# Kernel optimization log

Hardware: AMD Instinct MI355X
Metric: run time of the kernel (lower is better)

The kernel has to match this reference:

```python
import jax, jax.numpy as jnp
import numpy as np
from functools import partial

P = 7          # cfg.POOLING_SIZE
SAMP = 2       # fixed sampling ratio (torchvision sampling_ratio=0 is adaptive; fixed 2 used for jit)
IM_H, IM_W = 800.0, 1216.0


def conv2d(x, w, b, pad):
    y = jax.lax.conv_general_dilated(
        x, w, window_strides=(1, 1), padding=[(pad, pad), (pad, pad)],
        dimension_numbers=("NCHW", "OIHW", "NCHW"))
    return y + b[None, :, None, None]


def upsample_add(x, y):
    # F.upsample(x, size=(H,W), mode='bilinear') + y  (align_corners=False / half-pixel)
    return jax.image.resize(x, y.shape, method="bilinear") + y


def roi_align_level(feat, rois, scale):
    """torchvision roi_align (aligned=False) of all rois on one feature map.
    feat: [B,C,H,W]; rois: [N,5] = (batch_idx, x1,y1,x2,y2) in image coords.
    Returns [N,C,P,P]."""
    B, C, H, W = feat.shape
    Hf, Wf = float(H), float(W)

    def one(roi):
        b = roi[0].astype(jnp.int32)
        img = jnp.take(feat, b, axis=0)                       # [C,H,W]
        x1, y1, x2, y2 = roi[1] * scale, roi[2] * scale, roi[3] * scale, roi[4] * scale
        rw = jnp.maximum(x2 - x1, 1.0)
        rh = jnp.maximum(y2 - y1, 1.0)
        bh, bw = rh / P, rw / P
        # sample coords per bin: [P, SAMP] -> flat [P*SAMP]
        ys = (y1 + jnp.arange(P, dtype=feat.dtype)[:, None] * bh
              + (jnp.arange(SAMP, dtype=feat.dtype)[None, :] + 0.5) * bh / SAMP).reshape(-1)
        xs = (x1 + jnp.arange(P, dtype=feat.dtype)[:, None] * bw
              + (jnp.arange(SAMP, dtype=feat.dtype)[None, :] + 0.5) * bw / SAMP).reshape(-1)
        vy = (ys >= -1.0) & (ys <= Hf)
        vx = (xs >= -1.0) & (xs <= Wf)
        yc = jnp.clip(ys, 0.0, Hf - 1.0)
        xc = jnp.clip(xs, 0.0, Wf - 1.0)
        y0 = jnp.floor(yc).astype(jnp.int32)
        x0 = jnp.floor(xc).astype(jnp.int32)
        y1i = jnp.minimum(y0 + 1, H - 1)
        x1i = jnp.minimum(x0 + 1, W - 1)
        ly = yc - y0.astype(feat.dtype)
        lx = xc - x0.astype(feat.dtype)
        hy, hx = 1.0 - ly, 1.0 - lx
        v00 = img[:, y0[:, None], x0[None, :]]                # [C, PS, PS]
        v01 = img[:, y0[:, None], x1i[None, :]]
        v10 = img[:, y1i[:, None], x0[None, :]]
        v11 = img[:, y1i[:, None], x1i[None, :]]
        val = (hy[:, None] * hx[None, :]) * v00 + (hy[:, None] * lx[None, :]) * v01 \
            + (ly[:, None] * hx[None, :]) * v10 + (ly[:, None] * lx[None, :]) * v11
        val = val * (vy[:, None] & vx[None, :]).astype(feat.dtype)
        return val.reshape(C, P, SAMP, P, SAMP).mean(axis=(2, 4))   # [C,P,P]

    return jax.vmap(one)(rois)


def setup_inputs() -> dict:
    key = jax.random.key(0)
    ks = jax.random.split(key, 24)
    B = 2
    c2 = jax.random.normal(ks[0], (B, 256, 200, 304), jnp.float32)
    c3 = jax.random.normal(ks[1], (B, 512, 100, 152), jnp.float32)
    c4 = jax.random.normal(ks[2], (B, 1024, 50, 76), jnp.float32)
    c5 = jax.random.normal(ks[3], (B, 2048, 25, 38), jnp.float32)
    # FPN params (all project to 256 channels)
    def w(k, o, i, s):
        return jax.random.normal(k, (o, i, s, s), jnp.float32) * 0.01
    w_top, b_top = w(ks[4], 256, 2048, 1), jnp.zeros((256,), jnp.float32)
    w_lat1, b_lat1 = w(ks[5], 256, 1024, 1), jnp.zeros((256,), jnp.float32)
    w_lat2, b_lat2 = w(ks[6], 256, 512, 1), jnp.zeros((256,), jnp.float32)
    w_lat3, b_lat3 = w(ks[7], 256, 256, 1), jnp.zeros((256,), jnp.float32)
    w_sm1, b_sm1 = w(ks[8], 256, 256, 3), jnp.zeros((256,), jnp.float32)
    w_sm2, b_sm2 = w(ks[9], 256, 256, 3), jnp.zeros((256,), jnp.float32)
    w_sm3, b_sm3 = w(ks[10], 256, 256, 3), jnp.zeros((256,), jnp.float32)
    # ROIs: batch idx + boxes with log-uniform sizes spanning pyramid levels 2..5
    N = 1024
    bidx = jax.random.randint(ks[11], (N,), 0, B).astype(jnp.float32)
    size = jnp.exp(jax.random.uniform(ks[12], (N,), jnp.float32,
                                      np.log(32.0), np.log(640.0)))
    ar = jnp.exp(jax.random.uniform(ks[13], (N,), jnp.float32,
                                    np.log(0.5), np.log(2.0)))
    bw_ = jnp.minimum(size * jnp.sqrt(ar), IM_W - 1)
    bh_ = jnp.minimum(size / jnp.sqrt(ar), IM_H - 1)
    x1 = jax.random.uniform(ks[14], (N,), jnp.float32) * (IM_W - bw_)
    y1 = jax.random.uniform(ks[15], (N,), jnp.float32) * (IM_H - bh_)
    rois = jnp.stack([bidx, x1, y1, x1 + bw_, y1 + bh_], axis=1)
    im_info = jnp.array([[IM_H, IM_W, 1.0]], jnp.float32)
    return dict(c2=c2, c3=c3, c4=c4, c5=c5, rois=rois, im_info=im_info,
                w_top=w_top, b_top=b_top, w_lat1=w_lat1, b_lat1=b_lat1,
                w_lat2=w_lat2, b_lat2=b_lat2, w_lat3=w_lat3, b_lat3=b_lat3,
                w_sm1=w_sm1, b_sm1=b_sm1, w_sm2=w_sm2, b_sm2=b_sm2,
                w_sm3=w_sm3, b_sm3=b_sm3)


def reference(c2, c3, c4, c5, rois, im_info,
              w_top, b_top, w_lat1, b_lat1, w_lat2, b_lat2, w_lat3, b_lat3,
              w_sm1, b_sm1, w_sm2, b_sm2, w_sm3, b_sm3):
    # --- FPN top-down pathway ---
    p5 = conv2d(c5, w_top, b_top, 0)
    p4 = conv2d(upsample_add(p5, conv2d(c4, w_lat1, b_lat1, 0)), w_sm1, b_sm1, 1)
    p3 = conv2d(upsample_add(p4, conv2d(c3, w_lat2, b_lat2, 0)), w_sm2, b_sm2, 1)
    p2 = conv2d(upsample_add(p3, conv2d(c2, w_lat3, b_lat3, 0)), w_sm3, b_sm3, 1)
    mrcnn_feats = [p2, p3, p4, p5]
    # --- _PyramidRoI_Feat (POOLING_MODE == 'align') ---
    h = rois[:, 4] - rois[:, 2] + 1.0
    w_ = rois[:, 3] - rois[:, 1] + 1.0
    lvl = jnp.round(jnp.log(jnp.sqrt(h * w_) / 224.0) + 4.0)
    lvl = jnp.clip(lvl, 2.0, 5.0)
    im_h = im_info[0, 0]
    N, C = rois.shape[0], p2.shape[1]
    out = jnp.zeros((N, C, P, P), p2.dtype)
    for i, l in enumerate(range(2, 6)):
        scale = mrcnn_feats[i].shape[2] / im_h
        feat_l = roi_align_level(mrcnn_feats[i], rois, scale)
        out = jnp.where((lvl == l)[:, None, None, None], feat_l, out)
    return out
```

## Files before the change

### kernel.cpp

```cpp
#include <hip/hip_runtime.h>
#include <math.h>

typedef __attribute__((ext_vector_type(8))) short short8;
typedef __attribute__((ext_vector_type(4))) float f32x4;
typedef __attribute__((ext_vector_type(8))) unsigned short ushort8v;

__device__ __forceinline__ ushort f2bf(float f) {
    unsigned u = __builtin_bit_cast(unsigned, f);
    u = (u + 0x7fffu + ((u >> 16) & 1u)) >> 16;
    return (ushort)u;
}
__device__ __forceinline__ float bf2f(ushort h) {
    unsigned u = ((unsigned)h) << 16;
    return __builtin_bit_cast(float, u);
}

__device__ __forceinline__ void cp16(const ushort* g, ushort* l) {
    __builtin_amdgcn_global_load_lds(
        (const __attribute__((address_space(1))) unsigned int*)g,
        (__attribute__((address_space(3))) unsigned int*)l, 16, 0, 0);
}

__device__ __forceinline__ void pair_decode(int bid, int nt, int& tile, int& mm) {
    int f16 = (nt * 2) & ~15;
    if (bid < f16) { tile = ((bid >> 4) << 3) | (bid & 7); mm = (bid >> 3) & 1; }
    else { int r = bid - f16; tile = (f16 >> 1) + (r >> 1); mm = r & 1; }
}


__global__ void nchw2nhwc(const float* __restrict__ in, ushort* __restrict__ out,
                          int C, int HW)
{
    __shared__ float tile[32][33];
    const int n  = blockIdx.z;
    const int c0 = blockIdx.y * 32;
    const int p0 = blockIdx.x * 32;
    const float* inp = in + (size_t)n * C * HW;
    ushort* op = out + (size_t)n * HW * C;
    const int tx = threadIdx.x & 31, ty = threadIdx.x >> 5;
    #pragma unroll
    for (int i = 0; i < 4; ++i) {
        int c = ty + i * 8;
        int p = p0 + tx;
        tile[c][tx] = (p < HW) ? inp[(size_t)(c0 + c) * HW + p] : 0.f;
    }
    __syncthreads();
    #pragma unroll
    for (int i = 0; i < 4; ++i) {
        int p = ty + i * 8;
        if (p0 + p < HW) op[(size_t)(p0 + p) * C + c0 + tx] = f2bf(tile[tx][p]);
    }
}

__global__ void cast_k(const float* __restrict__ in, ushort* __restrict__ out, int n)
{
    int i = blockIdx.x * 256 + threadIdx.x;
    if (i < n) out[i] = f2bf(in[i]);
}

__global__ void pack_w3(const float* __restrict__ w, ushort* __restrict__ wp, int Cin)
{
    int i = blockIdx.x * 256 + threadIdx.x;
    int total = 256 * Cin * 9;
    if (i >= total) return;
    int co  = i / (9 * Cin);
    int rem = i - co * 9 * Cin;
    int tap = rem / Cin;
    int ci  = rem - tap * Cin;
    wp[i] = f2bf(w[(size_t)co * Cin * 9 + (size_t)ci * 9 + tap]);
}

__global__ void zero_border(ushort* __restrict__ T, int Hp, int Wp, int NB, int total)
{
    int i = blockIdx.x * 256 + threadIdx.x;
    if (i >= total) return;
    const int cg = (i & 31) * 8;
    const int pb = i >> 5;
    const int n  = pb / NB;
    const int b  = pb - n * NB;
    int y, x;
    if (b < 2 * Wp) { y = (b < Wp) ? 0 : (Hp - 1); x = (b < Wp) ? b : (b - Wp); }
    else { int rem = b - 2 * Wp; y = 1 + (rem >> 1); x = (rem & 1) ? (Wp - 1) : 0; }
    ushort8v z = {0, 0, 0, 0, 0, 0, 0, 0};
    *(ushort8v*)&T[((size_t)n * Hp * Wp + (size_t)y * Wp + x) * 256 + cg] = z;
}

template<int PADOUT>
__global__ __launch_bounds__(256, 4) void conv1_mfma(
    const ushort* __restrict__ X, const ushort* __restrict__ Wt,
    const float* __restrict__ bias, ushort* __restrict__ Y,
    int Cin, int H, int Wd, int nP)
{
    const int HW = H * Wd;
    int tile, mm;
    pair_decode(blockIdx.x, nP, tile, mm);
    const int p0 = tile * 128;
    const int m0 = mm << 7;
    const int n  = blockIdx.z;
    const ushort* Xn = X + (size_t)n * HW * Cin;

    const int t    = threadIdx.x;
    const int lane = t & 63;
    const int wave = t >> 6;
    const int l15  = lane & 15, lq = lane >> 4;

    __shared__ __align__(16) ushort smem[17408];

    const int rA  = ((t >> 6) << 4) | (t & 15);
    const int lq8 = ((t >> 4) & 3) * 8;
    const ushort* agA = Wt + (size_t)(m0 + rA) * Cin + lq8;
    const ushort* agB = agA + (size_t)64 * Cin;
    const ushort* XqA = Xn + (size_t)(p0 + rA) * Cin + lq8;
    const ushort* XqB = Xn + (size_t)(p0 + rA + 64) * Cin + lq8;

    const int fr    = (lq * 16 + l15) * 8;
    const int aoff  = ((wave >> 1) * 4) * 512;
    const int boff  = 4096 + ((wave & 1) * 4) * 512;
    const int wbase = wave << 9;

    const int nch = Cin >> 5;

    auto stage = [&](int bb, int c) {
        const int kA = c << 5;
        cp16(agA + kA, &smem[bb + wbase]);
        cp16(agB + kA, &smem[bb + 2048 + wbase]);
        cp16(XqA + kA, &smem[bb + 4096 + wbase]);
        cp16(XqB + kA, &smem[bb + 6144 + wbase]);
    };

    f32x4 acc[4][4] = {};

    stage(0, 0);
    __syncthreads();

    #pragma unroll 1
    for (int c = 0; c < nch; c += 2) {
        {
            stage(8192, c + 1);
            short8 af[4], bf[4];
            #pragma unroll
            for (int mi = 0; mi < 4; ++mi) af[mi] = *(const short8*)&smem[aoff + mi * 512 + fr];
            #pragma unroll
            for (int ni = 0; ni < 4; ++ni) bf[ni] = *(const short8*)&smem[boff + ni * 512 + fr];
            #pragma unroll
            for (int mi = 0; mi < 4; ++mi)
                #pragma unroll
                for (int ni = 0; ni < 4; ++ni)
                    acc[mi][ni] = __builtin_amdgcn_mfma_f32_16x16x32_bf16(
                        af[mi], bf[ni], acc[mi][ni], 0, 0, 0);
            __syncthreads();
        }
        {
            if (c + 2 < nch) stage(0, c + 2);
            short8 af[4], bf[4];
            #pragma unroll
            for (int mi = 0; mi < 4; ++mi) af[mi] = *(const short8*)&smem[8192 + aoff + mi * 512 + fr];
            #pragma unroll
            for (int ni = 0; ni < 4; ++ni) bf[ni] = *(const short8*)&smem[8192 + boff + ni * 512 + fr];
            #pragma unroll
            for (int mi = 0; mi < 4; ++mi)
                #pragma unroll
                for (int ni = 0; ni < 4; ++ni)
                    acc[mi][ni] = __builtin_amdgcn_mfma_f32_16x16x32_bf16(
                        af[mi], bf[ni], acc[mi][ni], 0, 0, 0);
            __syncthreads();
        }
    }

    const int wm = (wave >> 1) * 64, wn = (wave & 1) * 64;
    #pragma unroll
    for (int mi = 0; mi < 4; ++mi) {
        const int co = wm + mi * 16 + lq * 4;
        float4 bv = *(const float4*)&bias[m0 + co];
        float bb4[4] = {bv.x, bv.y, bv.z, bv.w};
        #pragma unroll
        for (int ni = 0; ni < 4; ++ni) {
            const int p = wn + ni * 16 + l15;
            ushort4 h;
            h.x = f2bf(acc[mi][ni][0] + bb4[0]);
            h.y = f2bf(acc[mi][ni][1] + bb4[1]);
            h.z = f2bf(acc[mi][ni][2] + bb4[2]);
            h.w = f2bf(acc[mi][ni][3] + bb4[3]);
            *(ushort4*)&smem[p * 136 + co] = h;
        }
    }
    __syncthreads();

    ushort* Yn = PADOUT ? (Y + (size_t)n * (H + 2) * (Wd + 2) * 256)
                        : (Y + (size_t)n * HW * 256);
    #pragma unroll
    for (int it = 0; it < 8; ++it) {
        int idx = it * 256 + t;
        int px  = idx >> 4;
        int off = (idx & 15) * 8;
        int qq  = p0 + px;
        if (qq >= HW) continue;
        uint4 v = *(const uint4*)&smem[px * 136 + off];
        if (PADOUT) {
            int y = qq / Wd, x = qq - (qq / Wd) * Wd;
            *(uint4*)&Yn[((size_t)(y + 1) * (Wd + 2) + (x + 1)) * 256 + m0 + off] = v;
        } else {
            *(uint4*)&Yn[(size_t)qq * 256 + m0 + off] = v;
        }
    }
}

__global__ __launch_bounds__(256, 4) void conv3_mfma(
    const ushort* __restrict__ X, const ushort* __restrict__ Wt,
    const float* __restrict__ bias, ushort* __restrict__ Y,
    int Hout, int Wout, int ct, int nt)
{
    const int Wp = Wout + 2;
    int tile, mm;
    pair_decode(blockIdx.x, nt, tile, mm);
    const int ty = tile / ct, tx = tile - ty * ct;
    int y0 = ty * 8;  if (y0 > Hout - 8)  y0 = Hout - 8;
    int x0 = tx * 16; if (x0 > Wout - 16) x0 = Wout - 16;
    const int m0 = mm << 7;
    const int nb = blockIdx.z;
    const ushort* Xn = X + (size_t)nb * (Hout + 2) * Wp * 256;

    const int t    = threadIdx.x;
    const int lane = t & 63;
    const int wave = t >> 6;
    const int l15  = lane & 15, lq = lane >> 4;

    __shared__ __align__(16) ushort smem[19712];
    const int A0o = 0, A1o = 4096, B0o = 8192, B1o = 13952;

    const int rA  = ((t >> 6) << 4) | (t & 15);
    const int lq8 = ((t >> 4) & 3) * 8;
    const ushort* agA = Wt + (size_t)(m0 + rA) * 2304 + lq8;
    const ushort* agB = agA + (size_t)64 * 2304;

    const int fr   = (lq * 16 + l15) * 8;
    const int aoff = (wave >> 1) * 2048;
    const int bb   = (((wave & 1) * 16 + lq) * 144) + l15 * 8;

    auto stageA = [&](int ab, int cc, int tap) {
        const int kA = tap * 256 + (cc << 5);
        cp16(agA + kA, &smem[ab + t * 8]);
        cp16(agB + kA, &smem[ab + 2048 + t * 8]);
    };
    auto stageB = [&](int bbuf, int cc) {
        const int cb = cc << 5;
        #pragma unroll
        for (int rnd = 0; rnd < 3; ++rnd) {
            int s = rnd * 256 + t;
            if (s < 720) {
                int py  = s / 72, rem = s - py * 72;
                int lqq = rem / 18, pxc = rem - lqq * 18;
                cp16(Xn + ((size_t)(y0 + py) * Wp + (x0 + pxc)) * 256 + cb + lqq * 8,
                     &smem[bbuf + s * 8]);
            }
        }
    };

    f32x4 acc[4][4] = {};

    stageB(B0o, 0);
    stageA(A0o, 0, 0);
    __syncthreads();

    #pragma unroll 1
    for (int cc = 0; cc < 8; ++cc) {
        const int pb = cc & 1;
        const int Bb = pb ? B1o : B0o;
        #pragma unroll
        for (int tap = 0; tap < 9; ++tap) {
            const int pa = pb ^ (tap & 1);
            const int Ab = pa ? A1o : A0o;
            const int An = pa ? A0o : A1o;
            if (tap < 8) stageA(An, cc, tap + 1);
            else if (cc < 7) { stageB(pb ? B0o : B1o, cc + 1); stageA(An, cc + 1, 0); }
            const int dy = tap / 3, dx = tap - dy * 3;
            short8 af[4], bf[4];
            #pragma unroll
            for (int mi = 0; mi < 4; ++mi) af[mi] = *(const short8*)&smem[Ab + aoff + mi * 512 + fr];
            #pragma unroll
            for (int ni = 0; ni < 4; ++ni) bf[ni] = *(const short8*)&smem[Bb + bb + (ni + dy) * 576 + dx * 8];
            #pragma unroll
            for (int mi = 0; mi < 4; ++mi)
                #pragma unroll
                for (int ni = 0; ni < 4; ++ni)
                    acc[mi][ni] = __builtin_amdgcn_mfma_f32_16x16x32_bf16(
                        af[mi], bf[ni], acc[mi][ni], 0, 0, 0);
            __syncthreads();
        }
    }

    const int wm = (wave >> 1) * 64, wn = (wave & 1) * 64;
    #pragma unroll
    for (int mi = 0; mi < 4; ++mi) {
        const int co = wm + mi * 16 + lq * 4;
        float4 bv = *(const float4*)&bias[m0 + co];
        float bb4[4] = {bv.x, bv.y, bv.z, bv.w};
        #pragma unroll
        for (int ni = 0; ni < 4; ++ni) {
            const int p = wn + ni * 16 + l15;
            ushort4 h;
            h.x = f2bf(acc[mi][ni][0] + bb4[0]);
            h.y = f2bf(acc[mi][ni][1] + bb4[1]);
            h.z = f2bf(acc[mi][ni][2] + bb4[2]);
            h.w = f2bf(acc[mi][ni][3] + bb4[3]);
            *(ushort4*)&smem[p * 136 + co] = h;
        }
    }
    __syncthreads();

    ushort* Yn = Y + (size_t)nb * Hout * Wout * 256;
    #pragma unroll
    for (int it = 0; it < 8; ++it) {
        int idx = it * 256 + t;
        int p   = idx >> 4;
        int off = (idx & 15) * 8;
        int yy  = y0 + (p >> 4), xx = x0 + (p & 15);
        *(uint4*)&Yn[((size_t)yy * Wout + xx) * 256 + m0 + off] =
            *(const uint4*)&smem[p * 136 + off];
    }
}

__global__ void upsample_add_nhwc(ushort* __restrict__ T, const ushort* __restrict__ Pn,
                                  int H, int Wd, int total32)
{
    int i = blockIdx.x * 256 + threadIdx.x;
    if (i >= total32) return;
    const int cg = (i & 31) * 8;
    const int q  = i >> 5;
    const int HW = H * Wd;
    const int n   = q / HW;
    const int pix = q - n * HW;
    const int y = pix / Wd, x = pix - (pix / Wd) * Wd;
    const int Hh = H >> 1, Wh = Wd >> 1;

    float sy = fminf(fmaxf(y * 0.5f - 0.25f, 0.f), (float)(Hh - 1));
    float sx = fminf(fmaxf(x * 0.5f - 0.25f, 0.f), (float)(Wh - 1));
    int y0 = (int)sy, x0 = (int)sx;
    int y1 = min(y0 + 1, Hh - 1), x1 = min(x0 + 1, Wh - 1);
    float fy = sy - (float)y0, fx = sx - (float)x0;

    const ushort* base = Pn + (size_t)n * Hh * Wh * 256 + cg;
    ushort8v a00 = *(const ushort8v*)&base[(size_t)(y0 * Wh + x0) * 256];
    ushort8v a01 = *(const ushort8v*)&base[(size_t)(y0 * Wh + x1) * 256];
    ushort8v a10 = *(const ushort8v*)&base[(size_t)(y1 * Wh + x0) * 256];
    ushort8v a11 = *(const ushort8v*)&base[(size_t)(y1 * Wh + x1) * 256];

    const int Wp2 = Wd + 2;
    ushort* tp = T + ((size_t)n * (H + 2) * Wp2 + (size_t)(y + 1) * Wp2 + (x + 1)) * 256 + cg;
    ushort8v tv = *(ushort8v*)tp;
    ushort8v r;
    #pragma unroll
    for (int j = 0; j < 8; ++j) {
        float v = (1.f - fy) * ((1.f - fx) * bf2f(a00[j]) + fx * bf2f(a01[j]))
                +        fy  * ((1.f - fx) * bf2f(a10[j]) + fx * bf2f(a11[j]));
        r[j] = f2bf(bf2f(tv[j]) + v);
    }
    *(ushort8v*)tp = r;
}

__global__ __launch_bounds__(256) void roi_align_k(
    const float* __restrict__ rois, const float* __restrict__ im_info,
    const ushort* __restrict__ p2, const ushort* __restrict__ p3,
    const ushort* __restrict__ p4, const ushort* __restrict__ p5,
    float* __restrict__ out)
{
    const int r   = blockIdx.x;
    const int tid = threadIdx.x;

    __shared__ int   s_y0[14], s_y1[14], s_x0[14], s_x1[14];
    __shared__ float s_ly[14], s_lx[14], s_vy[14], s_vx[14];
    __shared__ float s_o[256 * 49];

    const float bx  = rois[r * 5 + 0];
    const float x1r = rois[r * 5 + 1];
    const float y1r = rois[r * 5 + 2];
    const float x2r = rois[r * 5 + 3];
    const float y2r = rois[r * 5 + 4];

    const float hh = y2r - y1r + 1.f;
    const float ww = x2r - x1r + 1.f;
    float lf = rintf(logf(sqrtf(hh * ww) * (1.f / 224.f)) + 4.f);
    lf = fminf(fmaxf(lf, 2.f), 5.f);
    const int lvl = (int)lf;

    const ushort* feat; int H, W;
    if      (lvl == 2) { feat = p2; H = 200; W = 304; }
    else if (lvl == 3) { feat = p3; H = 100; W = 152; }
    else if (lvl == 4) { feat = p4; H = 50;  W = 76;  }
    else               { feat = p5; H = 25;  W = 38;  }

    const float im_h  = im_info[0];
    const float scale = (float)H / im_h;
    const float x1 = x1r * scale, y1 = y1r * scale;
    const float x2 = x2r * scale, y2 = y2r * scale;
    const float rw = fmaxf(x2 - x1, 1.f);
    const float rh = fmaxf(y2 - y1, 1.f);
    const float bh = rh * (1.f / 7.f);
    const float bw = rw * (1.f / 7.f);

    if (tid < 28) {
        if (tid < 14) {
            int i = tid, pi = i >> 1, s = i & 1;
            float ys = y1 + pi * bh + (s + 0.5f) * bh * 0.5f;
            float v  = (ys >= -1.f && ys <= (float)H) ? 1.f : 0.f;
            float yc = fminf(fmaxf(ys, 0.f), (float)H - 1.f);
            int y0 = (int)floorf(yc);
            s_y0[i] = y0; s_y1[i] = min(y0 + 1, H - 1);
            s_ly[i] = yc - (float)y0; s_vy[i] = v;
        } else {
            int i = tid - 14, pi = i >> 1, s = i & 1;
            float xs = x1 + pi * bw + (s + 0.5f) * bw * 0.5f;
            float v  = (xs >= -1.f && xs <= (float)W) ? 1.f : 0.f;
            float xc = fminf(fmaxf(xs, 0.f), (float)W - 1.f);
            int x0 = (int)floorf(xc);
            s_x0[i] = x0; s_x1[i] = min(x0 + 1, W - 1);
            s_lx[i] = xc - (float)x0; s_vx[i] = v;
        }
    }
    __syncthreads();

    const int b = (int)bx;
    const ushort* fc = feat + (size_t)b * H * W * 256 + tid;

    #pragma unroll
    for (int py = 0; py < 7; ++py) {
        #pragma unroll
        for (int px = 0; px < 7; ++px) {
            float acc = 0.f;
            #pragma unroll
            for (int sy = 0; sy < 2; ++sy) {
                #pragma unroll
                for (int sx = 0; sx < 2; ++sx) {
                    int iy = py * 2 + sy, ix = px * 2 + sx;
                    float ly = s_ly[iy], lx = s_lx[ix];
                    float hy = 1.f - ly, hx = 1.f - lx;
                    int y0 = s_y0[iy], y1i = s_y1[iy];
                    int x0 = s_x0[ix], x1i = s_x1[ix];
                    float v00 = bf2f(fc[(size_t)(y0 * W + x0) * 256]);
                    float v01 = bf2f(fc[(size_t)(y0 * W + x1i) * 256]);
                    float v10 = bf2f(fc[(size_t)(y1i * W + x0) * 256]);
                    float v11 = bf2f(fc[(size_t)(y1i * W + x1i) * 256]);
                    float val = hy * hx * v00 + hy * lx * v01
                              + ly * hx * v10 + ly * lx * v11;
                    acc += val * s_vy[iy] * s_vx[ix];
                }
            }
            s_o[tid * 49 + py * 7 + px] = acc * 0.25f;
        }
    }
    __syncthreads();
    float* orow = out + (size_t)r * 256 * 49;
    for (int it = 0; it < 49; ++it)
        orow[it * 256 + tid] = s_o[it * 256 + tid];
}

static inline int cdiv(int a, int b) { return (a + b - 1) / b; }

extern "C" void kernel_launch(void* const* d_in, const int* in_sizes, int n_in,
                              void* d_out, int out_size, void* d_ws, size_t ws_size,
                              hipStream_t stream) {
    const float* c2      = (const float*)d_in[0];
    const float* c3      = (const float*)d_in[1];
    const float* c4      = (const float*)d_in[2];
    const float* c5      = (const float*)d_in[3];
    const float* rois    = (const float*)d_in[4];
    const float* im_info = (const float*)d_in[5];
    const float* w_top   = (const float*)d_in[6];
    const float* b_top   = (const float*)d_in[7];
    const float* w_lat1  = (const float*)d_in[8];
    const float* b_lat1  = (const float*)d_in[9];
    const float* w_lat2  = (const float*)d_in[10];
    const float* b_lat2  = (const float*)d_in[11];
    const float* w_lat3  = (const float*)d_in[12];
    const float* b_lat3  = (const float*)d_in[13];
    const float* w_sm1   = (const float*)d_in[14];
    const float* b_sm1   = (const float*)d_in[15];
    const float* w_sm2   = (const float*)d_in[16];
    const float* b_sm2   = (const float*)d_in[17];
    const float* w_sm3   = (const float*)d_in[18];
    const float* b_sm3   = (const float*)d_in[19];
    float* out = (float*)d_out;
    ushort* ws = (ushort*)d_ws;

    ushort* c2t = ws;
    ushort* c3t = c2t + 31129600;
    ushort* c4t = c3t + 15564800;
    ushort* c5t = c4t + 7782400;
    ushort* p5  = c5t + 3891200;
    ushort* p4  = p5  + 486400;
    ushort* p3  = p4  + 1945600;
    ushort* T   = p3  + 7782400;
    ushort* wtp = T   + 31647744;
    ushort* wl1 = wtp + 524288;
    ushort* wl2 = wl1 + 262144;
    ushort* wl3 = wl2 + 131072;
    ushort* ws1 = wl3 + 65536;
    ushort* ws2 = ws1 + 589824;
    ushort* ws3 = ws2 + 589824;
    ushort* p2  = c2t;

    dim3 blk(256);

    cast_k<<<cdiv(524288, 256), blk, 0, stream>>>(w_top,  wtp, 524288);
    cast_k<<<cdiv(262144, 256), blk, 0, stream>>>(w_lat1, wl1, 262144);
    cast_k<<<cdiv(131072, 256), blk, 0, stream>>>(w_lat2, wl2, 131072);
    cast_k<<<cdiv(65536,  256), blk, 0, stream>>>(w_lat3, wl3, 65536);
    pack_w3<<<cdiv(589824, 256), blk, 0, stream>>>(w_sm1, ws1, 256);
    pack_w3<<<cdiv(589824, 256), blk, 0, stream>>>(w_sm2, ws2, 256);
    pack_w3<<<cdiv(589824, 256), blk, 0, stream>>>(w_sm3, ws3, 256);

    nchw2nhwc<<<dim3(1900, 8,  2), blk, 0, stream>>>(c2, c2t, 256,  60800);
    nchw2nhwc<<<dim3(475, 16,  2), blk, 0, stream>>>(c3, c3t, 512,  15200);
    nchw2nhwc<<<dim3(119, 32,  2), blk, 0, stream>>>(c4, c4t, 1024, 3800);
    nchw2nhwc<<<dim3(30,  64,  2), blk, 0, stream>>>(c5, c5t, 2048, 950);

    conv1_mfma<0><<<dim3(16, 1, 2), blk, 0, stream>>>(c5t, wtp, b_top, p5, 2048, 25, 38, 8);

    conv1_mfma<1><<<dim3(60, 1, 2), blk, 0, stream>>>(c4t, wl1, b_lat1, T, 1024, 50, 76, 30);
    zero_border<<<cdiv(16384, 256), blk, 0, stream>>>(T, 52, 78, 256, 16384);
    upsample_add_nhwc<<<cdiv(2 * 3800 * 32, 256), blk, 0, stream>>>(T, p5, 50, 76, 2 * 3800 * 32);
    conv3_mfma<<<dim3(70, 1, 2), blk, 0, stream>>>(T, ws1, b_sm1, p4, 50, 76, 5, 35);

    conv1_mfma<1><<<dim3(238, 1, 2), blk, 0, stream>>>(c3t, wl2, b_lat2, T, 512, 100, 152, 119);
    zero_border<<<cdiv(32512, 256), blk, 0, stream>>>(T, 102, 154, 508, 32512);
    upsample_add_nhwc<<<cdiv(2 * 15200 * 32, 256), blk, 0, stream>>>(T, p4, 100, 152, 2 * 15200 * 32);
    conv3_mfma<<<dim3(260, 1, 2), blk, 0, stream>>>(T, ws2, b_sm2, p3, 100, 152, 10, 130);

    conv1_mfma<1><<<dim3(950, 1, 2), blk, 0, stream>>>(c2t, wl3, b_lat3, T, 256, 200, 304, 475);
    zero_border<<<cdiv(64768, 256), blk, 0, stream>>>(T, 202, 306, 1012, 64768);
    upsample_add_nhwc<<<cdiv(2 * 60800 * 32, 256), blk, 0, stream>>>(T, p3, 200, 304, 2 * 60800 * 32);
    conv3_mfma<<<dim3(950, 1, 2), blk, 0, stream>>>(T, ws3, b_sm3, p2, 200, 304, 19, 475);

    roi_align_k<<<dim3(1024), blk, 0, stream>>>(rois, im_info, p2, p3, p4, p5, out);
}
```

Measured before the change: 1.024 ms.

## Triple-buffer conv3 weight ring with split B staging and widen NHWC transpose tiles

The 3x3 conv kernel now uses a three-slot ring for weight tiles with a prefetch distance of two taps. Activation staging is split across three taps, and barriers wait on partial vmcnt so loads overlap more MFMA work. It also XOR-swizzles the A tile rows to reduce LDS bank conflicts, raises MFMA wave priority, and lowers the occupancy bound to 3 to make room for the larger LDS footprint. The NCHW-to-NHWC transpose now handles 256 channels per block and writes paired bf16 values, giving fewer blocks and wider stores.

```diff
diff --git a/kernel.cpp b/kernel.cpp
--- a/kernel.cpp
+++ b/kernel.cpp
@@ -21,6 +21,8 @@
         (__attribute__((address_space(3))) unsigned int*)l, 16, 0, 0);
 }
 
+#define BARv(N) asm volatile("s_waitcnt vmcnt(" #N ") lgkmcnt(0)\n\ts_barrier" ::: "memory")
+
 __device__ __forceinline__ void pair_decode(int bid, int nt, int& tile, int& mm) {
     int f16 = (nt * 2) & ~15;
     if (bid < f16) { tile = ((bid >> 4) << 3) | (bid & 7); mm = (bid >> 3) & 1; }
@@ -28,27 +30,35 @@
 }
 
 
-__global__ void nchw2nhwc(const float* __restrict__ in, ushort* __restrict__ out,
-                          int C, int HW)
-{
-    __shared__ float tile[32][33];
+__global__ __launch_bounds__(256) void nchw2nhwc(const float* __restrict__ in,
+                                                 ushort* __restrict__ out,
+                                                 int C, int HW)
+{
+    __shared__ float tile[256][33];
     const int n  = blockIdx.z;
-    const int c0 = blockIdx.y * 32;
-    const int p0 = blockIdx.x * 32;
-    const float* inp = in + (size_t)n * C * HW;
-    ushort* op = out + (size_t)n * HW * C;
-    const int tx = threadIdx.x & 31, ty = threadIdx.x >> 5;
-    #pragma unroll
-    for (int i = 0; i < 4; ++i) {
-        int c = ty + i * 8;
-        int p = p0 + tx;
-        tile[c][tx] = (p < HW) ? inp[(size_t)(c0 + c) * HW + p] : 0.f;
-    }
-    __syncthreads();
-    #pragma unroll
-    for (int i = 0; i < 4; ++i) {
-        int p = ty + i * 8;
-        if (p0 + p < HW) op[(size_t)(p0 + p) * C + c0 + tx] = f2bf(tile[tx][p]);
+    const int c0 = blockIdx.y << 8;
+    const int p0 = blockIdx.x << 5;
+    const float* inp = in + (size_t)n * C * HW + (size_t)c0 * HW + p0;
+    const int t = threadIdx.x;
+    const int pr = t & 31, cr = t >> 5;
+    const bool pok = (p0 + pr) < HW;
+    #pragma unroll 8
+    for (int i = 0; i < 32; ++i) {
+        int c = i * 8 + cr;
+        tile[c][pr] = pok ? inp[(size_t)c * HW + pr] : 0.f;
+    }
+    __syncthreads();
+    ushort* op = out + (size_t)n * HW * C + c0;
+    const int cp = (t & 127) * 2, ph = t >> 7;
+    #pragma unroll 4
+    for (int j = 0; j < 16; ++j) {
+        int p = j * 2 + ph;
+        if (p0 + p < HW) {
+            ushort2 v;
+            v.x = f2bf(tile[cp][p]);
+            v.y = f2bf(tile[cp + 1][p]);
+            *(ushort2*)&op[(size_t)(p0 + p) * C + cp] = v;
+        }
     }
 }
 
@@ -205,7 +215,7 @@
     }
 }
 
-__global__ __launch_bounds__(256, 4) void conv3_mfma(
+__global__ __launch_bounds__(256, 3) void conv3_mfma(
     const ushort* __restrict__ X, const ushort* __restrict__ Wt,
     const float* __restrict__ bias, ushort* __restrict__ Y,
     int Hout, int Wout, int ct, int nt)
@@ -225,69 +235,76 @@
     const int wave = t >> 6;
     const int l15  = lane & 15, lq = lane >> 4;
 
-    __shared__ __align__(16) ushort smem[19712];
-    const int A0o = 0, A1o = 4096, B0o = 8192, B1o = 13952;
-
-    const int rA  = ((t >> 6) << 4) | (t & 15);
+    __shared__ __align__(16) ushort smem[23808];
+
+    const int rSw = ((t >> 6) << 4) | ((t & 15) ^ (((t >> 4) & 3) << 1));
     const int lq8 = ((t >> 4) & 3) * 8;
-    const ushort* agA = Wt + (size_t)(m0 + rA) * 2304 + lq8;
+    const ushort* agA = Wt + (size_t)(m0 + rSw) * 2304 + lq8;
     const ushort* agB = agA + (size_t)64 * 2304;
 
-    const int fr   = (lq * 16 + l15) * 8;
+    const int fra  = (lq * 16 + (l15 ^ (lq << 1))) * 8;
     const int aoff = (wave >> 1) * 2048;
     const int bb   = (((wave & 1) * 16 + lq) * 144) + l15 * 8;
 
-    auto stageA = [&](int ab, int cc, int tap) {
-        const int kA = tap * 256 + (cc << 5);
-        cp16(agA + kA, &smem[ab + t * 8]);
-        cp16(agB + kA, &smem[ab + 2048 + t * 8]);
+    auto stageA = [&](int ring, int ccA, int tapA) {
+        const int kA = tapA * 256 + (ccA << 5);
+        cp16(agA + kA, &smem[ring * 4096 + t * 8]);
+        cp16(agB + kA, &smem[ring * 4096 + 2048 + t * 8]);
     };
-    auto stageB = [&](int bbuf, int cc) {
+    auto stageBr = [&](int bsel, int cc, int rnd) {
         const int cb = cc << 5;
-        #pragma unroll
-        for (int rnd = 0; rnd < 3; ++rnd) {
-            int s = rnd * 256 + t;
-            if (s < 720) {
-                int py  = s / 72, rem = s - py * 72;
-                int lqq = rem / 18, pxc = rem - lqq * 18;
-                cp16(Xn + ((size_t)(y0 + py) * Wp + (x0 + pxc)) * 256 + cb + lqq * 8,
-                     &smem[bbuf + s * 8]);
-            }
+        int s = rnd * 256 + t;
+        if (s < 720) {
+            int py  = s / 72, rem = s - py * 72;
+            int lqq = rem / 18, pxc = rem - lqq * 18;
+            cp16(Xn + ((size_t)(y0 + py) * Wp + (x0 + pxc)) * 256 + cb + lqq * 8,
+                 &smem[12288 + bsel * 5760 + s * 8]);
         }
     };
 
     f32x4 acc[4][4] = {};
 
-    stageB(B0o, 0);
-    stageA(A0o, 0, 0);
+#define FRAG_MFMA(RING, BSEL, DY, DX)                                             \
+    {                                                                             \
+        short8 af[4], bf[4];                                                      \
+        _Pragma("unroll")                                                         \
+        for (int mi = 0; mi < 4; ++mi)                                            \
+            af[mi] = *(const short8*)&smem[(RING) * 4096 + aoff + mi * 512 + fra];\
+        _Pragma("unroll")                                                         \
+        for (int ni = 0; ni < 4; ++ni)                                            \
+            bf[ni] = *(const short8*)&smem[12288 + (BSEL) * 5760 + bb             \
+                                           + (ni + (DY)) * 576 + (DX) * 8];       \
+        __builtin_amdgcn_s_setprio(1);                                            \
+        _Pragma("unroll")                                                         \
+        for (int mi = 0; mi < 4; ++mi)                                            \
+            _Pragma("unroll")                                                     \
+            for (int ni = 0; ni < 4; ++ni)                                        \
+                acc[mi][ni] = __builtin_amdgcn_mfma_f32_16x16x32_bf16(            \
+                    af[mi], bf[ni], acc[mi][ni], 0, 0, 0);                        \
+        __builtin_amdgcn_s_setprio(0);                                            \
+    }
+
+    stageBr(0, 0, 0); stageBr(0, 0, 1); stageBr(0, 0, 2);
+    stageA(0, 0, 0);
+    stageA(1, 0, 1);
     __syncthreads();
 
     #pragma unroll 1
     for (int cc = 0; cc < 8; ++cc) {
-        const int pb = cc & 1;
-        const int Bb = pb ? B1o : B0o;
-        #pragma unroll
-        for (int tap = 0; tap < 9; ++tap) {
-            const int pa = pb ^ (tap & 1);
-            const int Ab = pa ? A1o : A0o;
-            const int An = pa ? A0o : A1o;
-            if (tap < 8) stageA(An, cc, tap + 1);
-            else if (cc < 7) { stageB(pb ? B0o : B1o, cc + 1); stageA(An, cc + 1, 0); }
-            const int dy = tap / 3, dx = tap - dy * 3;
-            short8 af[4], bf[4];
-            #pragma unroll
-            for (int mi = 0; mi < 4; ++mi) af[mi] = *(const short8*)&smem[Ab + aoff + mi * 512 + fr];
-            #pragma unroll
-            for (int ni = 0; ni < 4; ++ni) bf[ni] = *(const short8*)&smem[Bb + bb + (ni + dy) * 576 + dx * 8];
-            #pragma unroll
-            for (int mi = 0; mi < 4; ++mi)
-                #pragma unroll
-                for (int ni = 0; ni < 4; ++ni)
-                    acc[mi][ni] = __builtin_amdgcn_mfma_f32_16x16x32_bf16(
-                        af[mi], bf[ni], acc[mi][ni], 0, 0, 0);
-            __syncthreads();
-        }
-    }
+        const int bsel = cc & 1;
+        const int ccn  = (cc < 7) ? cc + 1 : 7;
+        stageA(2, cc, 2);                           FRAG_MFMA(0, bsel, 0, 0); BARv(2);
+        stageA(0, cc, 3); stageBr(bsel ^ 1, ccn, 0); FRAG_MFMA(1, bsel, 0, 1); BARv(3);
+        stageA(1, cc, 4); stageBr(bsel ^ 1, ccn, 1); FRAG_MFMA(2, bsel, 0, 2); BARv(3);
+        stageA(2, cc, 5); stageBr(bsel ^ 1, ccn, 2); FRAG_MFMA(0, bsel, 1, 0); BARv(3);
+        stageA(0, cc, 6);                           FRAG_MFMA(1, bsel, 1, 1); BARv(2);
+        stageA(1, cc, 7);                           FRAG_MFMA(2, bsel, 1, 2); BARv(2);
+        stageA(2, cc, 8);                           FRAG_MFMA(0, bsel, 2, 0); BARv(2);
+        stageA(0, ccn, 0);                          FRAG_MFMA(1, bsel, 2, 1); BARv(2);
+        stageA(1, ccn, 1);                          FRAG_MFMA(2, bsel, 2, 2); BARv(2);
+    }
+#undef FRAG_MFMA
+    __syncthreads();
 
     const int wm = (wave >> 1) * 64, wn = (wave & 1) * 64;
     #pragma unroll
@@ -509,10 +526,10 @@
     pack_w3<<<cdiv(589824, 256), blk, 0, stream>>>(w_sm2, ws2, 256);
     pack_w3<<<cdiv(589824, 256), blk, 0, stream>>>(w_sm3, ws3, 256);
 
-    nchw2nhwc<<<dim3(1900, 8,  2), blk, 0, stream>>>(c2, c2t, 256,  60800);
-    nchw2nhwc<<<dim3(475, 16,  2), blk, 0, stream>>>(c3, c3t, 512,  15200);
-    nchw2nhwc<<<dim3(119, 32,  2), blk, 0, stream>>>(c4, c4t, 1024, 3800);
-    nchw2nhwc<<<dim3(30,  64,  2), blk, 0, stream>>>(c5, c5t, 2048, 950);
+    nchw2nhwc<<<dim3(1900, 1, 2), blk, 0, stream>>>(c2, c2t, 256,  60800);
+    nchw2nhwc<<<dim3(475,  2, 2), blk, 0, stream>>>(c3, c3t, 512,  15200);
+    nchw2nhwc<<<dim3(119,  4, 2), blk, 0, stream>>>(c4, c4t, 1024, 3800);
+    nchw2nhwc<<<dim3(30,   8, 2), blk, 0, stream>>>(c5, c5t, 2048, 950);
 
     conv1_mfma<0><<<dim3(16, 1, 2), blk, 0, stream>>>(c5t, wtp, b_top, p5, 2048, 25, 38, 8);
 
```

Measured after the change: 1.052 ms. 2.7% more time.

## Fuse upsample-add into lateral conv epilogue and batch prep kernels

Applied to the files above, without the earlier changes.

The bilinear upsample-add now runs inside the 1x1 lateral conv epilogue, which removes a separate pass that read and wrote the padded T buffer. Weight casts, 3x3 weight packing and border zeroing are merged into one launch, and the four NCHW-to-NHWC transposes become one launch that uses 256-channel tiles and paired bf16 stores. To allow border zeroing up front, each level now gets its own padded buffer, which uses more workspace. The lateral output is also rounded to bf16 before the add, as it was before.

```diff
diff --git a/kernel.cpp b/kernel.cpp
--- a/kernel.cpp
+++ b/kernel.cpp
@@ -27,68 +27,101 @@
     else { int r = bid - f16; tile = (f16 >> 1) + (r >> 1); mm = r & 1; }
 }
 
-
-__global__ void nchw2nhwc(const float* __restrict__ in, ushort* __restrict__ out,
-                          int C, int HW)
+__global__ __launch_bounds__(256) void pack_zero_k(
+    const float* __restrict__ w_top,  const float* __restrict__ w_lat1,
+    const float* __restrict__ w_lat2, const float* __restrict__ w_lat3,
+    const float* __restrict__ w_sm1,  const float* __restrict__ w_sm2,
+    const float* __restrict__ w_sm3,
+    ushort* __restrict__ wtp, ushort* __restrict__ wl1,
+    ushort* __restrict__ wl2, ushort* __restrict__ wl3,
+    ushort* __restrict__ ws1, ushort* __restrict__ ws2, ushort* __restrict__ ws3,
+    ushort* __restrict__ T4, ushort* __restrict__ T3, ushort* __restrict__ T2)
 {
-    __shared__ float tile[32][33];
+    const int j = blockIdx.y;
+    const int i = blockIdx.x * 256 + threadIdx.x;
+    if (j < 4) {
+        const float* src; ushort* dst; int n;
+        if      (j == 0) { src = w_top;  dst = wtp; n = 524288; }
+        else if (j == 1) { src = w_lat1; dst = wl1; n = 262144; }
+        else if (j == 2) { src = w_lat2; dst = wl2; n = 131072; }
+        else             { src = w_lat3; dst = wl3; n = 65536;  }
+        if (i < n) dst[i] = f2bf(src[i]);
+    } else if (j < 7) {
+        const float* src; ushort* dst;
+        if      (j == 4) { src = w_sm1; dst = ws1; }
+        else if (j == 5) { src = w_sm2; dst = ws2; }
+        else             { src = w_sm3; dst = ws3; }
+        if (i < 589824) {
+            int co  = i / 2304;
+            int rem = i - co * 2304;
+            int tap = rem >> 8;
+            int ci  = rem & 255;
+            dst[i] = f2bf(src[(size_t)co * 2304 + (size_t)ci * 9 + tap]);
+        }
+    } else {
+        ushort* Tb; int Hp, Wp, NB, total;
+        if      (j == 7) { Tb = T4; Hp = 52;  Wp = 78;  NB = 256;  total = 16384; }
+        else if (j == 8) { Tb = T3; Hp = 102; Wp = 154; NB = 508;  total = 32512; }
+        else             { Tb = T2; Hp = 202; Wp = 306; NB = 1012; total = 64768; }
+        if (i < total) {
+            const int cg = (i & 31) * 8;
+            const int pb = i >> 5;
+            const int n  = pb / NB;
+            const int b  = pb - n * NB;
+            int y, x;
+            if (b < 2 * Wp) { y = (b < Wp) ? 0 : (Hp - 1); x = (b < Wp) ? b : (b - Wp); }
+            else { int rem = b - 2 * Wp; y = 1 + (rem >> 1); x = (rem & 1) ? (Wp - 1) : 0; }
+            ushort8v z = {0, 0, 0, 0, 0, 0, 0, 0};
+            *(ushort8v*)&Tb[((size_t)n * Hp * Wp + (size_t)y * Wp + x) * 256 + cg] = z;
+        }
+    }
+}
+
+__global__ __launch_bounds__(256) void nchw2nhwc_all(
+    const float* __restrict__ c2, const float* __restrict__ c3,
+    const float* __restrict__ c4, const float* __restrict__ c5,
+    ushort* __restrict__ c2t, ushort* __restrict__ c3t,
+    ushort* __restrict__ c4t, ushort* __restrict__ c5t)
+{
+    __shared__ float tile[256][33];
+    const int idx = blockIdx.x;
+    const float* in; ushort* out; int C, HW, tx, cy;
+    if (idx < 1900)      { in = c2; out = c2t; C = 256;  HW = 60800; tx = idx; cy = 0; }
+    else if (idx < 2850) { int l = idx - 1900; in = c3; out = c3t; C = 512;  HW = 15200; tx = l % 475; cy = l / 475; }
+    else if (idx < 3326) { int l = idx - 2850; in = c4; out = c4t; C = 1024; HW = 3800;  tx = l % 119; cy = l / 119; }
+    else                 { int l = idx - 3326; in = c5; out = c5t; C = 2048; HW = 950;   tx = l % 30;  cy = l / 30;  }
     const int n  = blockIdx.z;
-    const int c0 = blockIdx.y * 32;
-    const int p0 = blockIdx.x * 32;
-    const float* inp = in + (size_t)n * C * HW;
-    ushort* op = out + (size_t)n * HW * C;
-    const int tx = threadIdx.x & 31, ty = threadIdx.x >> 5;
-    #pragma unroll
-    for (int i = 0; i < 4; ++i) {
-        int c = ty + i * 8;
-        int p = p0 + tx;
-        tile[c][tx] = (p < HW) ? inp[(size_t)(c0 + c) * HW + p] : 0.f;
-    }
-    __syncthreads();
-    #pragma unroll
-    for (int i = 0; i < 4; ++i) {
-        int p = ty + i * 8;
-        if (p0 + p < HW) op[(size_t)(p0 + p) * C + c0 + tx] = f2bf(tile[tx][p]);
-    }
-}
-
-__global__ void cast_k(const float* __restrict__ in, ushort* __restrict__ out, int n)
-{
-    int i = blockIdx.x * 256 + threadIdx.x;
-    if (i < n) out[i] = f2bf(in[i]);
-}
-
-__global__ void pack_w3(const float* __restrict__ w, ushort* __restrict__ wp, int Cin)
-{
-    int i = blockIdx.x * 256 + threadIdx.x;
-    int total = 256 * Cin * 9;
-    if (i >= total) return;
-    int co  = i / (9 * Cin);
-    int rem = i - co * 9 * Cin;
-    int tap = rem / Cin;
-    int ci  = rem - tap * Cin;
-    wp[i] = f2bf(w[(size_t)co * Cin * 9 + (size_t)ci * 9 + tap]);
-}
-
-__global__ void zero_border(ushort* __restrict__ T, int Hp, int Wp, int NB, int total)
-{
-    int i = blockIdx.x * 256 + threadIdx.x;
-    if (i >= total) return;
-    const int cg = (i & 31) * 8;
-    const int pb = i >> 5;
-    const int n  = pb / NB;
-    const int b  = pb - n * NB;
-    int y, x;
-    if (b < 2 * Wp) { y = (b < Wp) ? 0 : (Hp - 1); x = (b < Wp) ? b : (b - Wp); }
-    else { int rem = b - 2 * Wp; y = 1 + (rem >> 1); x = (rem & 1) ? (Wp - 1) : 0; }
-    ushort8v z = {0, 0, 0, 0, 0, 0, 0, 0};
-    *(ushort8v*)&T[((size_t)n * Hp * Wp + (size_t)y * Wp + x) * 256 + cg] = z;
-}
-
-template<int PADOUT>
+    const int c0 = cy << 8;
+    const int p0 = tx << 5;
+    const float* inp = in + (size_t)n * C * HW + (size_t)c0 * HW + p0;
+    const int t = threadIdx.x;
+    const int pr = t & 31, cr = t >> 5;
+    const bool pok = (p0 + pr) < HW;
+    #pragma unroll 8
+    for (int i = 0; i < 32; ++i) {
+        int c = i * 8 + cr;
+        tile[c][pr] = pok ? inp[(size_t)c * HW + pr] : 0.f;
+    }
+    __syncthreads();
+    ushort* op = out + (size_t)n * HW * C + c0;
+    const int cp = (t & 127) * 2, ph = t >> 7;
+    #pragma unroll 4
+    for (int j = 0; j < 16; ++j) {
+        int p = j * 2 + ph;
+        if (p0 + p < HW) {
+            ushort2 v;
+            v.x = f2bf(tile[cp][p]);
+            v.y = f2bf(tile[cp + 1][p]);
+            *(ushort2*)&op[(size_t)(p0 + p) * C + cp] = v;
+        }
+    }
+}
+
+template<int UPADD>
 __global__ __launch_bounds__(256, 4) void conv1_mfma(
     const ushort* __restrict__ X, const ushort* __restrict__ Wt,
     const float* __restrict__ bias, ushort* __restrict__ Y,
+    const ushort* __restrict__ Pn,
     int Cin, int H, int Wd, int nP)
 {
     const int HW = H * Wd;
@@ -186,8 +219,8 @@
     }
     __syncthreads();
 
-    ushort* Yn = PADOUT ? (Y + (size_t)n * (H + 2) * (Wd + 2) * 256)
-                        : (Y + (size_t)n * HW * 256);
+    ushort* Yn = UPADD ? (Y + (size_t)n * (H + 2) * (Wd + 2) * 256)
+                       : (Y + (size_t)n * HW * 256);
     #pragma unroll
     for (int it = 0; it < 8; ++it) {
         int idx = it * 256 + t;
@@ -196,9 +229,29 @@
         int qq  = p0 + px;
         if (qq >= HW) continue;
         uint4 v = *(const uint4*)&smem[px * 136 + off];
-        if (PADOUT) {
-            int y = qq / Wd, x = qq - (qq / Wd) * Wd;
-            *(uint4*)&Yn[((size_t)(y + 1) * (Wd + 2) + (x + 1)) * 256 + m0 + off] = v;
+        if (UPADD) {
+            const int yq = qq / Wd, xq = qq - (qq / Wd) * Wd;
+            const int Hh = H >> 1, Wh = Wd >> 1;
+            float sy = fminf(fmaxf(yq * 0.5f - 0.25f, 0.f), (float)(Hh - 1));
+            float sx = fminf(fmaxf(xq * 0.5f - 0.25f, 0.f), (float)(Wh - 1));
+            int y0 = (int)sy, x0 = (int)sx;
+            int y1 = min(y0 + 1, Hh - 1), x1 = min(x0 + 1, Wh - 1);
+            float fy = sy - (float)y0, fx = sx - (float)x0;
+            const ushort* base = Pn + (size_t)n * Hh * Wh * 256 + m0 + off;
+            ushort8v a00 = *(const ushort8v*)&base[(size_t)(y0 * Wh + x0) * 256];
+            ushort8v a01 = *(const ushort8v*)&base[(size_t)(y0 * Wh + x1) * 256];
+            ushort8v a10 = *(const ushort8v*)&base[(size_t)(y1 * Wh + x0) * 256];
+            ushort8v a11 = *(const ushort8v*)&base[(size_t)(y1 * Wh + x1) * 256];
+            ushort8v tv = __builtin_bit_cast(ushort8v, v);
+            ushort8v r;
+            #pragma unroll
+            for (int jj = 0; jj < 8; ++jj) {
+                float up = (1.f - fy) * ((1.f - fx) * bf2f(a00[jj]) + fx * bf2f(a01[jj]))
+                         +        fy  * ((1.f - fx) * bf2f(a10[jj]) + fx * bf2f(a11[jj]));
+                r[jj] = f2bf(bf2f(tv[jj]) + up);
+            }
+            *(uint4*)&Yn[((size_t)(yq + 1) * (Wd + 2) + (xq + 1)) * 256 + m0 + off] =
+                __builtin_bit_cast(uint4, r);
         } else {
             *(uint4*)&Yn[(size_t)qq * 256 + m0 + off] = v;
         }
@@ -318,44 +371,6 @@
         *(uint4*)&Yn[((size_t)yy * Wout + xx) * 256 + m0 + off] =
             *(const uint4*)&smem[p * 136 + off];
     }
-}
-
-__global__ void upsample_add_nhwc(ushort* __restrict__ T, const ushort* __restrict__ Pn,
-                                  int H, int Wd, int total32)
-{
-    int i = blockIdx.x * 256 + threadIdx.x;
-    if (i >= total32) return;
-    const int cg = (i & 31) * 8;
-    const int q  = i >> 5;
-    const int HW = H * Wd;
-    const int n   = q / HW;
-    const int pix = q - n * HW;
-    const int y = pix / Wd, x = pix - (pix / Wd) * Wd;
-    const int Hh = H >> 1, Wh = Wd >> 1;
-
-    float sy = fminf(fmaxf(y * 0.5f - 0.25f, 0.f), (float)(Hh - 1));
-    float sx = fminf(fmaxf(x * 0.5f - 0.25f, 0.f), (float)(Wh - 1));
-    int y0 = (int)sy, x0 = (int)sx;
-    int y1 = min(y0 + 1, Hh - 1), x1 = min(x0 + 1, Wh - 1);
-    float fy = sy - (float)y0, fx = sx - (float)x0;
-
-    const ushort* base = Pn + (size_t)n * Hh * Wh * 256 + cg;
-    ushort8v a00 = *(const ushort8v*)&base[(size_t)(y0 * Wh + x0) * 256];
-    ushort8v a01 = *(const ushort8v*)&base[(size_t)(y0 * Wh + x1) * 256];
-    ushort8v a10 = *(const ushort8v*)&base[(size_t)(y1 * Wh + x0) * 256];
-    ushort8v a11 = *(const ushort8v*)&base[(size_t)(y1 * Wh + x1) * 256];
-
-    const int Wp2 = Wd + 2;
-    ushort* tp = T + ((size_t)n * (H + 2) * Wp2 + (size_t)(y + 1) * Wp2 + (x + 1)) * 256 + cg;
-    ushort8v tv = *(ushort8v*)tp;
-    ushort8v r;
-    #pragma unroll
-    for (int j = 0; j < 8; ++j) {
-        float v = (1.f - fy) * ((1.f - fx) * bf2f(a00[j]) + fx * bf2f(a01[j]))
-                +        fy  * ((1.f - fx) * bf2f(a10[j]) + fx * bf2f(a11[j]));
-        r[j] = f2bf(bf2f(tv[j]) + v);
-    }
-    *(ushort8v*)tp = r;
 }
 
 __global__ __launch_bounds__(256) void roi_align_k(
@@ -489,8 +504,10 @@
     ushort* p5  = c5t + 3891200;
     ushort* p4  = p5  + 486400;
     ushort* p3  = p4  + 1945600;
-    ushort* T   = p3  + 7782400;
-    ushort* wtp = T   + 31647744;
+    ushort* T2  = p3  + 7782400;
+    ushort* T3  = T2  + 31647744;
+    ushort* T4  = T3  + 8042496;
+    ushort* wtp = T4  + 2076672;
     ushort* wl1 = wtp + 524288;
     ushort* wl2 = wl1 + 262144;
     ushort* wl3 = wl2 + 131072;
@@ -501,35 +518,23 @@
 
     dim3 blk(256);
 
-    cast_k<<<cdiv(524288, 256), blk, 0, stream>>>(w_top,  wtp, 524288);
-    cast_k<<<cdiv(262144, 256), blk, 0, stream>>>(w_lat1, wl1, 262144);
-    cast_k<<<cdiv(131072, 256), blk, 0, stream>>>(w_lat2, wl2, 131072);
-    cast_k<<<cdiv(65536,  256), blk, 0, stream>>>(w_lat3, wl3, 65536);
-    pack_w3<<<cdiv(589824, 256), blk, 0, stream>>>(w_sm1, ws1, 256);
-    pack_w3<<<cdiv(589824, 256), blk, 0, stream>>>(w_sm2, ws2, 256);
-    pack_w3<<<cdiv(589824, 256), blk, 0, stream>>>(w_sm3, ws3, 256);
-
-    nchw2nhwc<<<dim3(1900, 8,  2), blk, 0, stream>>>(c2, c2t, 256,  60800);
-    nchw2nhwc<<<dim3(475, 16,  2), blk, 0, stream>>>(c3, c3t, 512,  15200);
-    nchw2nhwc<<<dim3(119, 32,  2), blk, 0, stream>>>(c4, c4t, 1024, 3800);
-    nchw2nhwc<<<dim3(30,  64,  2), blk, 0, stream>>>(c5, c5t, 2048, 950);
-
-    conv1_mfma<0><<<dim3(16, 1, 2), blk, 0, stream>>>(c5t, wtp, b_top, p5, 2048, 25, 38, 8);
-
-    conv1_mfma<1><<<dim3(60, 1, 2), blk, 0, stream>>>(c4t, wl1, b_lat1, T, 1024, 50, 76, 30);
-    zero_border<<<cdiv(16384, 256), blk, 0, stream>>>(T, 52, 78, 256, 16384);
-    upsample_add_nhwc<<<cdiv(2 * 3800 * 32, 256), blk, 0, stream>>>(T, p5, 50, 76, 2 * 3800 * 32);
-    conv3_mfma<<<dim3(70, 1, 2), blk, 0, stream>>>(T, ws1, b_sm1, p4, 50, 76, 5, 35);
-
-    conv1_mfma<1><<<dim3(238, 1, 2), blk, 0, stream>>>(c3t, wl2, b_lat2, T, 512, 100, 152, 119);
-    zero_border<<<cdiv(32512, 256), blk, 0, stream>>>(T, 102, 154, 508, 32512);
-    upsample_add_nhwc<<<cdiv(2 * 15200 * 32, 256), blk, 0, stream>>>(T, p4, 100, 152, 2 * 15200 * 32);
-    conv3_mfma<<<dim3(260, 1, 2), blk, 0, stream>>>(T, ws2, b_sm2, p3, 100, 152, 10, 130);
-
-    conv1_mfma<1><<<dim3(950, 1, 2), blk, 0, stream>>>(c2t, wl3, b_lat3, T, 256, 200, 304, 475);
-    zero_border<<<cdiv(64768, 256), blk, 0, stream>>>(T, 202, 306, 1012, 64768);
-    upsample_add_nhwc<<<cdiv(2 * 60800 * 32, 256), blk, 0, stream>>>(T, p3, 200, 304, 2 * 60800 * 32);
-    conv3_mfma<<<dim3(950, 1, 2), blk, 0, stream>>>(T, ws3, b_sm3, p2, 200, 304, 19, 475);
+    pack_zero_k<<<dim3(2304, 10), blk, 0, stream>>>(
+        w_top, w_lat1, w_lat2, w_lat3, w_sm1, w_sm2, w_sm3,
+        wtp, wl1, wl2, wl3, ws1, ws2, ws3, T4, T3, T2);
+
+    nchw2nhwc_all<<<dim3(3566, 1, 2), blk, 0, stream>>>(
+        c2, c3, c4, c5, c2t, c3t, c4t, c5t);
+
+    conv1_mfma<0><<<dim3(16, 1, 2), blk, 0, stream>>>(c5t, wtp, b_top, p5, (const ushort*)0, 2048, 25, 38, 8);
+
+    conv1_mfma<1><<<dim3(60, 1, 2), blk, 0, stream>>>(c4t, wl1, b_lat1, T4, p5, 1024, 50, 76, 30);
+    conv3_mfma<<<dim3(70, 1, 2), blk, 0, stream>>>(T4, ws1, b_sm1, p4, 50, 76, 5, 35);
+
+    conv1_mfma<1><<<dim3(238, 1, 2), blk, 0, stream>>>(c3t, wl2, b_lat2, T3, p4, 512, 100, 152, 119);
+    conv3_mfma<<<dim3(260, 1, 2), blk, 0, stream>>>(T3, ws2, b_sm2, p3, 100, 152, 10, 130);
+
+    conv1_mfma<1><<<dim3(950, 1, 2), blk, 0, stream>>>(c2t, wl3, b_lat3, T2, p3, 256, 200, 304, 475);
+    conv3_mfma<<<dim3(950, 1, 2), blk, 0, stream>>>(T2, ws3, b_sm3, p2, 200, 304, 19, 475);
 
     roi_align_k<<<dim3(1024), blk, 0, stream>>>(rois, im_info, p2, p3, p4, p5, out);
 }
```

Result: no change. 1.019 ms (-0.6%).
